# Kernel optimization log

Hardware: AMD Instinct MI355X
Metric: run time of the kernel (lower is better)

## Reference

```python
import jax, jax.numpy as jnp
import numpy as np

EMB = 64
N = 8192
G = 32
TMAX = 32


def _mlp(x, w1, b1, w2, b2, act=True):
    h = x @ w1 + b1
    if act:
        h = jnp.maximum(h, 0.0)
    return h @ w2 + b2


def setup_inputs() -> dict:
    key = jax.random.key(0)
    ks = jax.random.split(key, 10)
    s = 1.0 / np.sqrt(EMB)

    def rnd(k, shape, scale):
        return jax.random.normal(k, shape, dtype=jnp.float32) * np.float32(scale)

    return {
        # dense node-node adjacency; scaled so the 32-step recurrence stays tame
        "M_vv": jax.random.normal(ks[0], (N, N), dtype=jnp.float32) / np.float32(np.sqrt(N)),
        "segment_ids": jnp.repeat(jnp.arange(G, dtype=jnp.int32), N // G),  # graph id per node
        # v_init MLP (with_act=False -> purely linear)
        "vinit_w1": rnd(ks[1], (1, EMB), 1.0), "vinit_b1": jnp.zeros((EMB,), jnp.float32),
        "vinit_w2": rnd(ks[2], (EMB, EMB), s), "vinit_b2": jnp.zeros((EMB,), jnp.float32),
        # mlpV (Linear-ReLU-Linear)
        "mlpv_w1": rnd(ks[3], (EMB, EMB), s), "mlpv_b1": jnp.zeros((EMB,), jnp.float32),
        "mlpv_w2": rnd(ks[4], (EMB, EMB), s), "mlpv_b2": jnp.zeros((EMB,), jnp.float32),
        # nn.RNN(emb, emb) cell params
        "rnn_wih": rnd(ks[5], (EMB, EMB), s), "rnn_whh": rnd(ks[6], (EMB, EMB), s),
        "rnn_bih": jnp.zeros((EMB,), jnp.float32), "rnn_bhh": jnp.zeros((EMB,), jnp.float32),
        # V_vote_mlp (emb -> emb -> 1)
        "vote_w1": rnd(ks[7], (EMB, EMB), s), "vote_b1": jnp.zeros((EMB,), jnp.float32),
        "vote_w2": rnd(ks[8], (EMB, 1), s), "vote_b2": jnp.zeros((1,), jnp.float32),
        "num_graphs": G,
    }


def reference(M_vv, segment_ids,
              vinit_w1, vinit_b1, vinit_w2, vinit_b2,
              mlpv_w1, mlpv_b1, mlpv_w2, mlpv_b2,
              rnn_wih, rnn_whh, rnn_bih, rnn_bhh,
              vote_w1, vote_b1, vote_w2, vote_b2,
              num_graphs):
    n = M_vv.shape[0]
    one = jnp.ones((1, 1), dtype=M_vv.dtype)
    v0 = _mlp(one, vinit_w1, vinit_b1, vinit_w2, vinit_b2, act=False)  # [1, E]
    V = jnp.broadcast_to(v0, (n, v0.shape[1]))  # expand over nodes
    h0 = jnp.zeros_like(V)

    def step(carry, _):
        V, h = carry
        x = _mlp(M_vv @ V, mlpv_w1, mlpv_b1, mlpv_w2, mlpv_b2)  # aggregate + MLP
        # nn.RNN (tanh) cell, seq_len=1: output == new hidden
        h_new = jnp.tanh(x @ rnn_wih.T + rnn_bih + h @ rnn_whh.T + rnn_bhh)
        return (h_new, h_new), None

    (V, _), _ = jax.lax.scan(step, (V, h0), None, length=TMAX)

    vote = _mlp(V, vote_w1, vote_b1, vote_w2, vote_b2)[:, 0]  # [N]
    sums = jax.ops.segment_sum(vote, segment_ids, num_segments=num_graphs)
    cnts = jax.ops.segment_sum(jnp.ones_like(vote), segment_ids, num_segments=num_graphs)
    means = sums / cnts                    # per-graph mean vote (split + mean)
    pred = jax.nn.sigmoid(means)           # per-graph prediction
    return pred, means, V
```

## Files before the change

### kernel.cpp

```cpp
#include <hip/hip_runtime.h>
#include <hip/hip_bf16.h>
#include <cmath>

#define NQ 8192
#define EMB 64
#define KSPLIT 16
#define KCHUNK (NQ / KSPLIT)
#define TMAX 32
#define MSCALE 256.0f
#define MINV (1.0f / 256.0f)
#define SUBK 64
#define BPAD 72

typedef __bf16 bf16x8 __attribute__((ext_vector_type(8)));
typedef _Float16 f16x8 __attribute__((ext_vector_type(8)));
typedef float f32x4 __attribute__((ext_vector_type(4)));

__global__ __launch_bounds__(256) void k_conv(const float* __restrict__ M,
                                              _Float16* __restrict__ Mh, long n) {
    long i = ((long)blockIdx.x * 256 + threadIdx.x) * 8;
    const long stride = (long)gridDim.x * 256 * 8;
    for (; i < n; i += stride) {
        float4 f0 = *(const float4*)(M + i);
        float4 f1 = *(const float4*)(M + i + 4);
        f16x8 o;
        o[0] = (_Float16)(f0.x * MSCALE); o[1] = (_Float16)(f0.y * MSCALE);
        o[2] = (_Float16)(f0.z * MSCALE); o[3] = (_Float16)(f0.w * MSCALE);
        o[4] = (_Float16)(f1.x * MSCALE); o[5] = (_Float16)(f1.y * MSCALE);
        o[6] = (_Float16)(f1.z * MSCALE); o[7] = (_Float16)(f1.w * MSCALE);
        *(f16x8*)(Mh + i) = o;
    }
}

__global__ __launch_bounds__(256) void k_wprep(
    const float* __restrict__ vi_w1, const float* __restrict__ vi_b1,
    const float* __restrict__ vi_w2, const float* __restrict__ vi_b2,
    const float* __restrict__ w1, const float* __restrict__ w2,
    const float* __restrict__ wih, const float* __restrict__ whh,
    float* __restrict__ v0,
    __bf16* __restrict__ w1h, __bf16* __restrict__ w1l,
    __bf16* __restrict__ w2h, __bf16* __restrict__ w2l,
    __bf16* __restrict__ wihH, __bf16* __restrict__ wihL,
    __bf16* __restrict__ whhH, __bf16* __restrict__ whhL) {
    __shared__ float h[EMB];
    const int t = threadIdx.x;
    if (t < EMB) h[t] = vi_w1[t] + vi_b1[t];
    __syncthreads();
    if (t < EMB) {
        float s = vi_b2[t];
        for (int i = 0; i < EMB; ++i) s += h[i] * vi_w2[i * EMB + t];
        v0[t] = s;
    }
    for (int i = t; i < EMB * EMB; i += 256) {
        const int r = i >> 6, c = i & 63;
        float v;
        __bf16 hi;
        v = w1[c * EMB + r]; hi = (__bf16)v;
        w1h[i] = hi; w1l[i] = (__bf16)(v - (float)hi);
        v = w2[c * EMB + r]; hi = (__bf16)v;
        w2h[i] = hi; w2l[i] = (__bf16)(v - (float)hi);
        v = wih[i]; hi = (__bf16)v;
        wihH[i] = hi; wihL[i] = (__bf16)(v - (float)hi);
        v = whh[i]; hi = (__bf16)v;
        whhH[i] = hi; whhL[i] = (__bf16)(v - (float)hi);
    }
}

__global__ __launch_bounds__(256) void k_fill(const float* __restrict__ v0,
                                              _Float16* __restrict__ Vh,
                                              _Float16* __restrict__ Vl) {
    const int c = blockIdx.x;
    const float v = v0[c];
    const _Float16 hi = (_Float16)v;
    const _Float16 lo = (_Float16)(v - (float)hi);
    f16x8 oh = {hi, hi, hi, hi, hi, hi, hi, hi};
    f16x8 ol = {lo, lo, lo, lo, lo, lo, lo, lo};
    for (int i = threadIdx.x; i < NQ / 8; i += 256) {
        *(f16x8*)(Vh + (long)c * NQ + (long)i * 8) = oh;
        *(f16x8*)(Vl + (long)c * NQ + (long)i * 8) = ol;
    }
}

__global__ __launch_bounds__(256, 4) void k_gemm_big(
    const _Float16* __restrict__ A, const _Float16* __restrict__ Bh,
    const _Float16* __restrict__ Bl, float* __restrict__ P) {
    __shared__ _Float16 Bs[2][2][EMB][BPAD];
    const int ks   = blockIdx.x & (KSPLIT - 1);
    const int rt   = blockIdx.x / KSPLIT;
    const int t    = threadIdx.x;
    const int wave = t >> 6;
    const int lane = t & 63;
    const int l15  = lane & 15;
    const int kg   = lane >> 4;
    const int row0 = rt * 128 + wave * 32;
    const long kcb = (long)ks * KCHUNK;
    const _Float16* Ap0 = A + (long)(row0 + l15) * NQ + kcb + kg * 8;
    const _Float16* Ap1 = Ap0 + (long)16 * NQ;
    const int scol  = t >> 2;
    const int spart = (t & 3) * 16;
    const _Float16* gH = Bh + (long)scol * NQ + kcb + spart;
    const _Float16* gL = Bl + (long)scol * NQ + kcb + spart;

    f32x4 acc00 = {}, acc01 = {}, acc02 = {}, acc03 = {};
    f32x4 acc10 = {}, acc11 = {}, acc12 = {}, acc13 = {};

    f16x8 sh0 = *(const f16x8*)(gH);
    f16x8 sh1 = *(const f16x8*)(gH + 8);
    f16x8 sl0 = *(const f16x8*)(gL);
    f16x8 sl1 = *(const f16x8*)(gL + 8);
    *(f16x8*)&Bs[0][0][scol][spart]     = sh0;
    *(f16x8*)&Bs[0][0][scol][spart + 8] = sh1;
    *(f16x8*)&Bs[0][1][scol][spart]     = sl0;
    *(f16x8*)&Bs[0][1][scol][spart + 8] = sl1;
    __syncthreads();

#pragma unroll
    for (int sub = 0; sub < KCHUNK / SUBK; ++sub) {
        const int buf = sub & 1;
        if (sub < KCHUNK / SUBK - 1) {
            const long nk = (long)(sub + 1) * SUBK;
            sh0 = *(const f16x8*)(gH + nk);
            sh1 = *(const f16x8*)(gH + nk + 8);
            sl0 = *(const f16x8*)(gL + nk);
            sl1 = *(const f16x8*)(gL + nk + 8);
        }
#pragma unroll
        for (int it = 0; it < SUBK / 32; ++it) {
            const long ka = (long)sub * SUBK + it * 32;
            const int  kl = it * 32 + kg * 8;
            f16x8 a0 = *(const f16x8*)(Ap0 + ka);
            f16x8 a1 = *(const f16x8*)(Ap1 + ka);
            f16x8 bh0 = *(const f16x8*)&Bs[buf][0][0 * 16 + l15][kl];
            f16x8 bh1 = *(const f16x8*)&Bs[buf][0][1 * 16 + l15][kl];
            f16x8 bh2 = *(const f16x8*)&Bs[buf][0][2 * 16 + l15][kl];
            f16x8 bh3 = *(const f16x8*)&Bs[buf][0][3 * 16 + l15][kl];
            f16x8 bl0 = *(const f16x8*)&Bs[buf][1][0 * 16 + l15][kl];
            f16x8 bl1 = *(const f16x8*)&Bs[buf][1][1 * 16 + l15][kl];
            f16x8 bl2 = *(const f16x8*)&Bs[buf][1][2 * 16 + l15][kl];
            f16x8 bl3 = *(const f16x8*)&Bs[buf][1][3 * 16 + l15][kl];
            acc00 = __builtin_amdgcn_mfma_f32_16x16x32_f16(a0, bh0, acc00, 0, 0, 0);
            acc10 = __builtin_amdgcn_mfma_f32_16x16x32_f16(a1, bh0, acc10, 0, 0, 0);
            acc01 = __builtin_amdgcn_mfma_f32_16x16x32_f16(a0, bh1, acc01, 0, 0, 0);
            acc11 = __builtin_amdgcn_mfma_f32_16x16x32_f16(a1, bh1, acc11, 0, 0, 0);
            acc02 = __builtin_amdgcn_mfma_f32_16x16x32_f16(a0, bh2, acc02, 0, 0, 0);
            acc12 = __builtin_amdgcn_mfma_f32_16x16x32_f16(a1, bh2, acc12, 0, 0, 0);
            acc03 = __builtin_amdgcn_mfma_f32_16x16x32_f16(a0, bh3, acc03, 0, 0, 0);
            acc13 = __builtin_amdgcn_mfma_f32_16x16x32_f16(a1, bh3, acc13, 0, 0, 0);
            acc00 = __builtin_amdgcn_mfma_f32_16x16x32_f16(a0, bl0, acc00, 0, 0, 0);
            acc10 = __builtin_amdgcn_mfma_f32_16x16x32_f16(a1, bl0, acc10, 0, 0, 0);
            acc01 = __builtin_amdgcn_mfma_f32_16x16x32_f16(a0, bl1, acc01, 0, 0, 0);
            acc11 = __builtin_amdgcn_mfma_f32_16x16x32_f16(a1, bl1, acc11, 0, 0, 0);
            acc02 = __builtin_amdgcn_mfma_f32_16x16x32_f16(a0, bl2, acc02, 0, 0, 0);
            acc12 = __builtin_amdgcn_mfma_f32_16x16x32_f16(a1, bl2, acc12, 0, 0, 0);
            acc03 = __builtin_amdgcn_mfma_f32_16x16x32_f16(a0, bl3, acc03, 0, 0, 0);
            acc13 = __builtin_amdgcn_mfma_f32_16x16x32_f16(a1, bl3, acc13, 0, 0, 0);
        }
        if (sub < KCHUNK / SUBK - 1) {
            const int nb = buf ^ 1;
            *(f16x8*)&Bs[nb][0][scol][spart]     = sh0;
            *(f16x8*)&Bs[nb][0][scol][spart + 8] = sh1;
            *(f16x8*)&Bs[nb][1][scol][spart]     = sl0;
            *(f16x8*)&Bs[nb][1][scol][spart + 8] = sl1;
            __syncthreads();
        }
    }
    float* Pp = P + ((long)ks * NQ + row0) * EMB;
#pragma unroll
    for (int i = 0; i < 4; ++i) {
        const int r = kg * 4 + i;
        Pp[r * EMB +  0 + l15] = acc00[i];
        Pp[r * EMB + 16 + l15] = acc01[i];
        Pp[r * EMB + 32 + l15] = acc02[i];
        Pp[r * EMB + 48 + l15] = acc03[i];
        Pp[(16 + r) * EMB +  0 + l15] = acc10[i];
        Pp[(16 + r) * EMB + 16 + l15] = acc11[i];
        Pp[(16 + r) * EMB + 32 + l15] = acc12[i];
        Pp[(16 + r) * EMB + 48 + l15] = acc13[i];
    }
}

__device__ __forceinline__ void mmstage3(const __bf16* Ah, const __bf16* Al,
                                         const __bf16* Bh, const __bf16* Bl,
                                         int rloc, int l15, int kg, f32x4 acc[4],
                                         bool init) {
    if (init) { acc[0] = {}; acc[1] = {}; acc[2] = {}; acc[3] = {}; }
#pragma unroll
    for (int kk = 0; kk < EMB; kk += 32) {
        const int ka = kk + kg * 8;
        const int aidx = (rloc * EMB + ka) ^ ((rloc & 7) << 3);
        bf16x8 ah = *(const bf16x8*)&Ah[aidx];
        bf16x8 al = *(const bf16x8*)&Al[aidx];
#pragma unroll
        for (int ct = 0; ct < 4; ++ct) {
            bf16x8 bh = *(const bf16x8*)&Bh[(ct * 16 + l15) * EMB + ka];
            bf16x8 bl = *(const bf16x8*)&Bl[(ct * 16 + l15) * EMB + ka];
            acc[ct] = __builtin_amdgcn_mfma_f32_16x16x32_bf16(ah, bh, acc[ct], 0, 0, 0);
            acc[ct] = __builtin_amdgcn_mfma_f32_16x16x32_bf16(ah, bl, acc[ct], 0, 0, 0);
            acc[ct] = __builtin_amdgcn_mfma_f32_16x16x32_bf16(al, bh, acc[ct], 0, 0, 0);
        }
    }
}

#define SNODE 32
__global__ __launch_bounds__(128) void k_step(
    const float* __restrict__ P, const float* Hprev,
    const float* __restrict__ b1, const float* __restrict__ b2,
    const float* __restrict__ bih, const float* __restrict__ bhh,
    const __bf16* __restrict__ w1h, const __bf16* __restrict__ w1l,
    const __bf16* __restrict__ w2h, const __bf16* __restrict__ w2l,
    const __bf16* __restrict__ wihH, const __bf16* __restrict__ wihL,
    const __bf16* __restrict__ whhH, const __bf16* __restrict__ whhL,
    float* Vout, _Float16* __restrict__ Vth, _Float16* __restrict__ Vtl,
    int isFirst) {
    __shared__ __bf16 Ahi[SNODE * EMB], Alo[SNODE * EMB];
    __shared__ __bf16 Phi[SNODE * EMB], Plo[SNODE * EMB];
    __shared__ __bf16 Hhi[SNODE * EMB], Hlo[SNODE * EMB];
    __shared__ __bf16 Xhi[SNODE * EMB], Xlo[SNODE * EMB];
    const int t = threadIdx.x;
    const int base = blockIdx.x * SNODE;

    for (int i = t * 4; i < SNODE * EMB; i += 128 * 4) {
        const int node = i >> 6, col = i & 63;
        float4 s = {0.f, 0.f, 0.f, 0.f};
#pragma unroll
        for (int sp = 0; sp < KSPLIT; ++sp) {
            float4 pv = *(const float4*)&P[((long)sp * NQ + base + node) * EMB + col];
            s.x += pv.x; s.y += pv.y; s.z += pv.z; s.w += pv.w;
        }
        float4 hp = {0.f, 0.f, 0.f, 0.f};
        if (!isFirst) hp = *(const float4*)&Hprev[(long)(base + node) * EMB + col];
        const float sv[4] = {s.x * MINV, s.y * MINV, s.z * MINV, s.w * MINV};
        const float hv[4] = {hp.x, hp.y, hp.z, hp.w};
#pragma unroll
        for (int j = 0; j < 4; ++j) {
            const int sw = (i + j) ^ ((node & 7) << 3);
            __bf16 hi = (__bf16)sv[j];
            Ahi[sw] = hi; Alo[sw] = (__bf16)(sv[j] - (float)hi);
            hi = (__bf16)hv[j];
            Phi[sw] = hi; Plo[sw] = (__bf16)(hv[j] - (float)hi);
        }
    }
    __syncthreads();

    const int wave = t >> 6, lane = t & 63, l15 = lane & 15, kg = lane >> 4;
    const int rloc = wave * 16 + l15;
    f32x4 acc[4];

    mmstage3(Ahi, Alo, w1h, w1l, rloc, l15, kg, acc, true);
#pragma unroll
    for (int ct = 0; ct < 4; ++ct) {
        const int c = ct * 16 + l15;
        const float bc = b1[c];
#pragma unroll
        for (int i = 0; i < 4; ++i) {
            const int r = wave * 16 + kg * 4 + i;
            const float v = fmaxf(acc[ct][i] + bc, 0.f);
            const int sw = (r * EMB + c) ^ ((r & 7) << 3);
            __bf16 hi = (__bf16)v;
            Hhi[sw] = hi; Hlo[sw] = (__bf16)(v - (float)hi);
        }
    }
    __syncthreads();

    mmstage3(Hhi, Hlo, w2h, w2l, rloc, l15, kg, acc, true);
#pragma unroll
    for (int ct = 0; ct < 4; ++ct) {
        const int c = ct * 16 + l15;
        const float bc = b2[c];
#pragma unroll
        for (int i = 0; i < 4; ++i) {
            const int r = wave * 16 + kg * 4 + i;
            const float v = acc[ct][i] + bc;
            const int sw = (r * EMB + c) ^ ((r & 7) << 3);
            __bf16 hi = (__bf16)v;
            Xhi[sw] = hi; Xlo[sw] = (__bf16)(v - (float)hi);
        }
    }
    __syncthreads();

    mmstage3(Xhi, Xlo, wihH, wihL, rloc, l15, kg, acc, true);
    mmstage3(Phi, Plo, whhH, whhL, rloc, l15, kg, acc, false);
#pragma unroll
    for (int ct = 0; ct < 4; ++ct) {
        const int c = ct * 16 + l15;
        const float bc = bih[c] + bhh[c];
#pragma unroll
        for (int i = 0; i < 4; ++i) {
            const int r = wave * 16 + kg * 4 + i;
            const float v = tanhf(acc[ct][i] + bc);
            Vout[(long)(base + r) * EMB + c] = v;
            const _Float16 hi = (_Float16)v;
            Vth[(long)c * NQ + base + r] = hi;
            Vtl[(long)c * NQ + base + r] = (_Float16)(v - (float)hi);
        }
    }
}

__global__ __launch_bounds__(256) void k_vote(const float* __restrict__ V,
                                              const float* __restrict__ vw1,
                                              const float* __restrict__ vb1,
                                              const float* __restrict__ vw2,
                                              const float* __restrict__ vb2,
                                              float* __restrict__ out) {
    __shared__ float W1[EMB * EMB];
    __shared__ float red[256];
    const int g = blockIdx.x, t = threadIdx.x;
    for (int i = t; i < EMB * EMB; i += 256) W1[i] = vw1[i];
    __syncthreads();
    const int node = g * 256 + t;
    float a[EMB];
    const float4* vp4 = (const float4*)(V + (long)node * EMB);
#pragma unroll
    for (int k = 0; k < 16; ++k) {
        float4 f = vp4[k];
        a[4 * k] = f.x; a[4 * k + 1] = f.y; a[4 * k + 2] = f.z; a[4 * k + 3] = f.w;
    }
    float vote = vb2[0];
    for (int j = 0; j < EMB; ++j) {
        float h = vb1[j];
#pragma unroll
        for (int k = 0; k < EMB; ++k) h += a[k] * W1[k * EMB + j];
        vote += fmaxf(h, 0.f) * vw2[j];
    }
    red[t] = vote;
    __syncthreads();
    for (int s = 128; s > 0; s >>= 1) {
        if (t < s) red[t] += red[t + s];
        __syncthreads();
    }
    if (t == 0) {
        const float mean = red[0] / 256.f;
        out[g] = 1.f / (1.f + expf(-mean));
        out[32 + g] = mean;
    }
}

extern "C" void kernel_launch(void* const* d_in, const int* in_sizes, int n_in,
                              void* d_out, int out_size, void* d_ws, size_t ws_size,
                              hipStream_t stream) {
    const float* M     = (const float*)d_in[0];
    const float* vi_w1 = (const float*)d_in[2];
    const float* vi_b1 = (const float*)d_in[3];
    const float* vi_w2 = (const float*)d_in[4];
    const float* vi_b2 = (const float*)d_in[5];
    const float* m_w1  = (const float*)d_in[6];
    const float* m_b1  = (const float*)d_in[7];
    const float* m_w2  = (const float*)d_in[8];
    const float* m_b2  = (const float*)d_in[9];
    const float* r_wih = (const float*)d_in[10];
    const float* r_whh = (const float*)d_in[11];
    const float* r_bih = (const float*)d_in[12];
    const float* r_bhh = (const float*)d_in[13];
    const float* v_w1  = (const float*)d_in[14];
    const float* v_b1  = (const float*)d_in[15];
    const float* v_w2  = (const float*)d_in[16];
    const float* v_b2  = (const float*)d_in[17];

    float* out  = (float*)d_out;
    float* Vout = out + 64;

    char* p = (char*)d_ws;
    _Float16* Mh  = (_Float16*)p; p += (size_t)NQ * NQ * 2;
    float*    part = (float*)p;   p += (size_t)KSPLIT * NQ * EMB * 4;
    _Float16* Vth = (_Float16*)p; p += (size_t)EMB * NQ * 2;
    _Float16* Vtl = (_Float16*)p; p += (size_t)EMB * NQ * 2;
    __bf16* w1h  = (__bf16*)p; p += EMB * EMB * 2;
    __bf16* w1l  = (__bf16*)p; p += EMB * EMB * 2;
    __bf16* w2h  = (__bf16*)p; p += EMB * EMB * 2;
    __bf16* w2l  = (__bf16*)p; p += EMB * EMB * 2;
    __bf16* wihH = (__bf16*)p; p += EMB * EMB * 2;
    __bf16* wihL = (__bf16*)p; p += EMB * EMB * 2;
    __bf16* whhH = (__bf16*)p; p += EMB * EMB * 2;
    __bf16* whhL = (__bf16*)p; p += EMB * EMB * 2;
    float*  v0   = (float*)p;  p += EMB * 4;

    hipLaunchKernelGGL(k_conv, dim3(4096), dim3(256), 0, stream, M, Mh, (long)NQ * NQ);
    hipLaunchKernelGGL(k_wprep, dim3(1), dim3(256), 0, stream, vi_w1, vi_b1, vi_w2, vi_b2,
                       m_w1, m_w2, r_wih, r_whh, v0, w1h, w1l, w2h, w2l,
                       wihH, wihL, whhH, whhL);
    hipLaunchKernelGGL(k_fill, dim3(EMB), dim3(256), 0, stream, v0, Vth, Vtl);

    for (int t = 0; t < TMAX; ++t) {
        hipLaunchKernelGGL(k_gemm_big, dim3((NQ / 128) * KSPLIT), dim3(256), 0, stream,
                           Mh, Vth, Vtl, part);
        hipLaunchKernelGGL(k_step, dim3(NQ / SNODE), dim3(128), 0, stream, part, Vout,
                           m_b1, m_b2, r_bih, r_bhh, w1h, w1l, w2h, w2l,
                           wihH, wihL, whhH, whhL, Vout, Vth, Vtl,
                           t == 0 ? 1 : 0);
    }
    hipLaunchKernelGGL(k_vote, dim3(32), dim3(256), 0, stream, Vout, v_w1, v_b1, v_w2,
                       v_b2, out);
}
```

Measured before the change: 1.584 ms.

## Prefetch A fragments across sub-tiles in big GEMM and reshape step kernel to 16 nodes

In the big split-K GEMM, the A operand fragments for the next 64-wide sub-tile are now loaded into registers one iteration ahead, so global-load latency for M overlaps the MFMA work. The low-part B reads from LDS are also moved after the first MFMA batch. Separately, the step kernel now handles 16 nodes per block with 256 threads: all four waves share the P reduction, but only wave 0 runs the small MLP/RNN matmuls. The prefetch adds register pressure, and the step-kernel reshape leaves three waves idle during the matmul stages.

```diff
diff --git a/kernel.cpp b/kernel.cpp
--- a/kernel.cpp
+++ b/kernel.cpp
@@ -11,6 +11,7 @@
 #define MINV (1.0f / 256.0f)
 #define SUBK 64
 #define BPAD 72
+#define NSUB (KCHUNK / SUBK)
 
 typedef __bf16 bf16x8 __attribute__((ext_vector_type(8)));
 typedef _Float16 f16x8 __attribute__((ext_vector_type(8)));
@@ -108,6 +109,10 @@
     f16x8 sh1 = *(const f16x8*)(gH + 8);
     f16x8 sl0 = *(const f16x8*)(gL);
     f16x8 sl1 = *(const f16x8*)(gL + 8);
+    f16x8 a00 = *(const f16x8*)(Ap0);
+    f16x8 a10 = *(const f16x8*)(Ap1);
+    f16x8 a01 = *(const f16x8*)(Ap0 + 32);
+    f16x8 a11 = *(const f16x8*)(Ap1 + 32);
     *(f16x8*)&Bs[0][0][scol][spart]     = sh0;
     *(f16x8*)&Bs[0][0][scol][spart + 8] = sh1;
     *(f16x8*)&Bs[0][1][scol][spart]     = sl0;
@@ -115,29 +120,29 @@
     __syncthreads();
 
 #pragma unroll
-    for (int sub = 0; sub < KCHUNK / SUBK; ++sub) {
+    for (int sub = 0; sub < NSUB; ++sub) {
         const int buf = sub & 1;
-        if (sub < KCHUNK / SUBK - 1) {
+        f16x8 na00, na10, na01, na11;
+        if (sub < NSUB - 1) {
             const long nk = (long)(sub + 1) * SUBK;
             sh0 = *(const f16x8*)(gH + nk);
             sh1 = *(const f16x8*)(gH + nk + 8);
             sl0 = *(const f16x8*)(gL + nk);
             sl1 = *(const f16x8*)(gL + nk + 8);
-        }
-#pragma unroll
-        for (int it = 0; it < SUBK / 32; ++it) {
-            const long ka = (long)sub * SUBK + it * 32;
-            const int  kl = it * 32 + kg * 8;
-            f16x8 a0 = *(const f16x8*)(Ap0 + ka);
-            f16x8 a1 = *(const f16x8*)(Ap1 + ka);
+            na00 = *(const f16x8*)(Ap0 + nk);
+            na10 = *(const f16x8*)(Ap1 + nk);
+            na01 = *(const f16x8*)(Ap0 + nk + 32);
+            na11 = *(const f16x8*)(Ap1 + nk + 32);
+        }
+#pragma unroll
+        for (int it = 0; it < 2; ++it) {
+            const int kl = it * 32 + kg * 8;
+            const f16x8 a0 = it ? a01 : a00;
+            const f16x8 a1 = it ? a11 : a10;
             f16x8 bh0 = *(const f16x8*)&Bs[buf][0][0 * 16 + l15][kl];
             f16x8 bh1 = *(const f16x8*)&Bs[buf][0][1 * 16 + l15][kl];
             f16x8 bh2 = *(const f16x8*)&Bs[buf][0][2 * 16 + l15][kl];
             f16x8 bh3 = *(const f16x8*)&Bs[buf][0][3 * 16 + l15][kl];
-            f16x8 bl0 = *(const f16x8*)&Bs[buf][1][0 * 16 + l15][kl];
-            f16x8 bl1 = *(const f16x8*)&Bs[buf][1][1 * 16 + l15][kl];
-            f16x8 bl2 = *(const f16x8*)&Bs[buf][1][2 * 16 + l15][kl];
-            f16x8 bl3 = *(const f16x8*)&Bs[buf][1][3 * 16 + l15][kl];
             acc00 = __builtin_amdgcn_mfma_f32_16x16x32_f16(a0, bh0, acc00, 0, 0, 0);
             acc10 = __builtin_amdgcn_mfma_f32_16x16x32_f16(a1, bh0, acc10, 0, 0, 0);
             acc01 = __builtin_amdgcn_mfma_f32_16x16x32_f16(a0, bh1, acc01, 0, 0, 0);
@@ -146,6 +151,10 @@
             acc12 = __builtin_amdgcn_mfma_f32_16x16x32_f16(a1, bh2, acc12, 0, 0, 0);
             acc03 = __builtin_amdgcn_mfma_f32_16x16x32_f16(a0, bh3, acc03, 0, 0, 0);
             acc13 = __builtin_amdgcn_mfma_f32_16x16x32_f16(a1, bh3, acc13, 0, 0, 0);
+            f16x8 bl0 = *(const f16x8*)&Bs[buf][1][0 * 16 + l15][kl];
+            f16x8 bl1 = *(const f16x8*)&Bs[buf][1][1 * 16 + l15][kl];
+            f16x8 bl2 = *(const f16x8*)&Bs[buf][1][2 * 16 + l15][kl];
+            f16x8 bl3 = *(const f16x8*)&Bs[buf][1][3 * 16 + l15][kl];
             acc00 = __builtin_amdgcn_mfma_f32_16x16x32_f16(a0, bl0, acc00, 0, 0, 0);
             acc10 = __builtin_amdgcn_mfma_f32_16x16x32_f16(a1, bl0, acc10, 0, 0, 0);
             acc01 = __builtin_amdgcn_mfma_f32_16x16x32_f16(a0, bl1, acc01, 0, 0, 0);
@@ -155,13 +164,14 @@
             acc03 = __builtin_amdgcn_mfma_f32_16x16x32_f16(a0, bl3, acc03, 0, 0, 0);
             acc13 = __builtin_amdgcn_mfma_f32_16x16x32_f16(a1, bl3, acc13, 0, 0, 0);
         }
-        if (sub < KCHUNK / SUBK - 1) {
+        if (sub < NSUB - 1) {
             const int nb = buf ^ 1;
             *(f16x8*)&Bs[nb][0][scol][spart]     = sh0;
             *(f16x8*)&Bs[nb][0][scol][spart + 8] = sh1;
             *(f16x8*)&Bs[nb][1][scol][spart]     = sl0;
             *(f16x8*)&Bs[nb][1][scol][spart + 8] = sl1;
             __syncthreads();
+            a00 = na00; a10 = na10; a01 = na01; a11 = na11;
         }
     }
     float* Pp = P + ((long)ks * NQ + row0) * EMB;
@@ -201,8 +211,8 @@
     }
 }
 
-#define SNODE 32
-__global__ __launch_bounds__(128) void k_step(
+#define SNODE 16
+__global__ __launch_bounds__(256, 2) void k_step(
     const float* __restrict__ P, const float* Hprev,
     const float* __restrict__ b1, const float* __restrict__ b2,
     const float* __restrict__ bih, const float* __restrict__ bhh,
@@ -219,7 +229,7 @@
     const int t = threadIdx.x;
     const int base = blockIdx.x * SNODE;
 
-    for (int i = t * 4; i < SNODE * EMB; i += 128 * 4) {
+    for (int i = t * 4; i < SNODE * EMB; i += 256 * 4) {
         const int node = i >> 6, col = i & 63;
         float4 s = {0.f, 0.f, 0.f, 0.f};
 #pragma unroll
@@ -243,55 +253,61 @@
     __syncthreads();
 
     const int wave = t >> 6, lane = t & 63, l15 = lane & 15, kg = lane >> 4;
-    const int rloc = wave * 16 + l15;
+    const int rloc = l15;
     f32x4 acc[4];
 
-    mmstage3(Ahi, Alo, w1h, w1l, rloc, l15, kg, acc, true);
-#pragma unroll
-    for (int ct = 0; ct < 4; ++ct) {
-        const int c = ct * 16 + l15;
-        const float bc = b1[c];
-#pragma unroll
-        for (int i = 0; i < 4; ++i) {
-            const int r = wave * 16 + kg * 4 + i;
-            const float v = fmaxf(acc[ct][i] + bc, 0.f);
-            const int sw = (r * EMB + c) ^ ((r & 7) << 3);
-            __bf16 hi = (__bf16)v;
-            Hhi[sw] = hi; Hlo[sw] = (__bf16)(v - (float)hi);
-        }
-    }
-    __syncthreads();
-
-    mmstage3(Hhi, Hlo, w2h, w2l, rloc, l15, kg, acc, true);
-#pragma unroll
-    for (int ct = 0; ct < 4; ++ct) {
-        const int c = ct * 16 + l15;
-        const float bc = b2[c];
-#pragma unroll
-        for (int i = 0; i < 4; ++i) {
-            const int r = wave * 16 + kg * 4 + i;
-            const float v = acc[ct][i] + bc;
-            const int sw = (r * EMB + c) ^ ((r & 7) << 3);
-            __bf16 hi = (__bf16)v;
-            Xhi[sw] = hi; Xlo[sw] = (__bf16)(v - (float)hi);
-        }
-    }
-    __syncthreads();
-
-    mmstage3(Xhi, Xlo, wihH, wihL, rloc, l15, kg, acc, true);
-    mmstage3(Phi, Plo, whhH, whhL, rloc, l15, kg, acc, false);
-#pragma unroll
-    for (int ct = 0; ct < 4; ++ct) {
-        const int c = ct * 16 + l15;
-        const float bc = bih[c] + bhh[c];
-#pragma unroll
-        for (int i = 0; i < 4; ++i) {
-            const int r = wave * 16 + kg * 4 + i;
-            const float v = tanhf(acc[ct][i] + bc);
-            Vout[(long)(base + r) * EMB + c] = v;
-            const _Float16 hi = (_Float16)v;
-            Vth[(long)c * NQ + base + r] = hi;
-            Vtl[(long)c * NQ + base + r] = (_Float16)(v - (float)hi);
+    if (wave == 0) {
+        mmstage3(Ahi, Alo, w1h, w1l, rloc, l15, kg, acc, true);
+#pragma unroll
+        for (int ct = 0; ct < 4; ++ct) {
+            const int c = ct * 16 + l15;
+            const float bc = b1[c];
+#pragma unroll
+            for (int i = 0; i < 4; ++i) {
+                const int r = kg * 4 + i;
+                const float v = fmaxf(acc[ct][i] + bc, 0.f);
+                const int sw = (r * EMB + c) ^ ((r & 7) << 3);
+                __bf16 hi = (__bf16)v;
+                Hhi[sw] = hi; Hlo[sw] = (__bf16)(v - (float)hi);
+            }
+        }
+    }
+    __syncthreads();
+
+    if (wave == 0) {
+        mmstage3(Hhi, Hlo, w2h, w2l, rloc, l15, kg, acc, true);
+#pragma unroll
+        for (int ct = 0; ct < 4; ++ct) {
+            const int c = ct * 16 + l15;
+            const float bc = b2[c];
+#pragma unroll
+            for (int i = 0; i < 4; ++i) {
+                const int r = kg * 4 + i;
+                const float v = acc[ct][i] + bc;
+                const int sw = (r * EMB + c) ^ ((r & 7) << 3);
+                __bf16 hi = (__bf16)v;
+                Xhi[sw] = hi; Xlo[sw] = (__bf16)(v - (float)hi);
+            }
+        }
+    }
+    __syncthreads();
+
+    if (wave == 0) {
+        mmstage3(Xhi, Xlo, wihH, wihL, rloc, l15, kg, acc, true);
+        mmstage3(Phi, Plo, whhH, whhL, rloc, l15, kg, acc, false);
+#pragma unroll
+        for (int ct = 0; ct < 4; ++ct) {
+            const int c = ct * 16 + l15;
+            const float bc = bih[c] + bhh[c];
+#pragma unroll
+            for (int i = 0; i < 4; ++i) {
+                const int r = kg * 4 + i;
+                const float v = tanhf(acc[ct][i] + bc);
+                Vout[(long)(base + r) * EMB + c] = v;
+                const _Float16 hi = (_Float16)v;
+                Vth[(long)c * NQ + base + r] = hi;
+                Vtl[(long)c * NQ + base + r] = (_Float16)(v - (float)hi);
+            }
         }
     }
 }
@@ -383,7 +399,7 @@
     for (int t = 0; t < TMAX; ++t) {
         hipLaunchKernelGGL(k_gemm_big, dim3((NQ / 128) * KSPLIT), dim3(256), 0, stream,
                            Mh, Vth, Vtl, part);
-        hipLaunchKernelGGL(k_step, dim3(NQ / SNODE), dim3(128), 0, stream, part, Vout,
+        hipLaunchKernelGGL(k_step, dim3(NQ / SNODE), dim3(256), 0, stream, part, Vout,
                            m_b1, m_b2, r_bih, r_bhh, w1h, w1l, w2h, w2l,
                            wihH, wihL, whhH, whhL, Vout, Vth, Vtl,
                            t == 0 ? 1 : 0);
```

After: 1.513 ms (median of 2 runs). 4.5% less time.
